# Optimization experiments

Measured on AMD Instinct MI355X. Metric: run time of the kernel, lower is better.

The kernel has to match this reference:

```python
import jax, jax.numpy as jnp
import numpy as np

N, D = 65536, 2000


def setup_inputs() -> dict:
    key = jax.random.key(0)
    factor = jax.random.normal(key, (N, D), dtype=jnp.float32)
    weight = jnp.float32(0.01)
    return {"factor": factor, "weight": weight}


def reference(factor, weight):
    # trace(factor[1:] @ factor[:-1].T) == sum of row-wise dot products of
    # shifted rows; O(n*d) instead of the original's O(n^2*d) matmul.
    n = factor.shape[0]
    tr = jnp.sum(factor[1:] * factor[:-1])
    return -weight * tr / (n - 1)
```

## Files before the change

kernel.cpp:

```cpp
#include <hip/hip_runtime.h>


#define N_ROWS 65536
#define D_COLS 2000
#define NBLOCKS 2048
#define NTHREADS 256
#define CHUNK 16000LL

__global__ __launch_bounds__(NTHREADS) void shifted_dot_kernel(
    const float* __restrict__ a,
    const float* __restrict__ weight,
    float* __restrict__ out,
    long long total4) {
    const float4* a4 = (const float4*)a;
    const long long shift4 = D_COLS / 4;

    long long start = (long long)blockIdx.x * CHUNK;
    long long end   = start + CHUNK;
    if (end > total4) end = total4;

    float acc = 0.0f;
    for (long long k = start + threadIdx.x; k < end; k += NTHREADS) {
        float4 x = a4[k];
        float4 y = a4[k + shift4];
        acc += x.x * y.x + x.y * y.y + x.z * y.z + x.w * y.w;
    }

    #pragma unroll
    for (int off = 32; off > 0; off >>= 1)
        acc += __shfl_down(acc, off, 64);

    __shared__ float wave_sums[NTHREADS / 64];
    int lane = threadIdx.x & 63;
    int wid  = threadIdx.x >> 6;
    if (lane == 0) wave_sums[wid] = acc;
    __syncthreads();

    if (threadIdx.x == 0) {
        float s = wave_sums[0] + wave_sums[1] + wave_sums[2] + wave_sums[3];
        float w = weight[0];
        atomicAdd(out, s * (-w / (float)(N_ROWS - 1)));
    }
}

extern "C" void kernel_launch(void* const* d_in, const int* in_sizes, int n_in,
                              void* d_out, int out_size, void* d_ws, size_t ws_size,
                              hipStream_t stream) {
    const float* factor = (const float*)d_in[0];
    const float* weight = (const float*)d_in[1];
    float* out = (float*)d_out;

    hipMemsetAsync(out, 0, sizeof(float), stream);

    const long long total4 = (long long)(N_ROWS - 1) * D_COLS / 4;

    dim3 grid(NBLOCKS), block(NTHREADS);
    shifted_dot_kernel<<<grid, block, 0, stream>>>(factor, weight, out, total4);
}
```

Before: 686.0 us.

## Walk columns down row bands and reuse previous row in registers

```diff
diff --git a/kernel.cpp b/kernel.cpp
--- a/kernel.cpp
+++ b/kernel.cpp
@@ -3,43 +3,57 @@
 
 #define N_ROWS 65536
 #define D_COLS 2000
-#define NBLOCKS 2048
-#define NTHREADS 256
-#define CHUNK 16000LL
+#define NBLOCKS 1024
+#define NTHREADS 512
+#define ROWS_PER_BLOCK 64
 
-__global__ __launch_bounds__(NTHREADS) void shifted_dot_kernel(
+__global__ __launch_bounds__(NTHREADS) void shifted_dot_colwise(
     const float* __restrict__ a,
     const float* __restrict__ weight,
-    float* __restrict__ out,
-    long long total4) {
-    const float4* a4 = (const float4*)a;
-    const long long shift4 = D_COLS / 4;
+    float* __restrict__ out) {
+    const int t = threadIdx.x;
 
-    long long start = (long long)blockIdx.x * CHUNK;
-    long long end   = start + CHUNK;
-    if (end > total4) end = total4;
+    float4 acc = make_float4(0.f, 0.f, 0.f, 0.f);
 
-    float acc = 0.0f;
-    for (long long k = start + threadIdx.x; k < end; k += NTHREADS) {
-        float4 x = a4[k];
-        float4 y = a4[k + shift4];
-        acc += x.x * y.x + x.y * y.y + x.z * y.z + x.w * y.w;
+    if (t < D_COLS / 4) {
+        const int r0 = blockIdx.x * ROWS_PER_BLOCK;
+        int r1 = r0 + ROWS_PER_BLOCK;
+        if (r1 > N_ROWS - 1) r1 = N_ROWS - 1;
+
+        const float4* col = (const float4*)(a + (long long)r0 * D_COLS) + t;
+        const int row4 = D_COLS / 4;
+
+        float4 prev = col[0];
+        #pragma unroll 4
+        for (int n = r0 + 1; n <= r1; ++n) {
+            col += row4;
+            float4 curr = *col;
+            acc.x += prev.x * curr.x;
+            acc.y += prev.y * curr.y;
+            acc.z += prev.z * curr.z;
+            acc.w += prev.w * curr.w;
+            prev = curr;
+        }
     }
+
+    float s = acc.x + acc.y + acc.z + acc.w;
 
     #pragma unroll
     for (int off = 32; off > 0; off >>= 1)
-        acc += __shfl_down(acc, off, 64);
+        s += __shfl_down(s, off, 64);
 
     __shared__ float wave_sums[NTHREADS / 64];
-    int lane = threadIdx.x & 63;
-    int wid  = threadIdx.x >> 6;
-    if (lane == 0) wave_sums[wid] = acc;
+    int lane = t & 63;
+    int wid  = t >> 6;
+    if (lane == 0) wave_sums[wid] = s;
     __syncthreads();
 
-    if (threadIdx.x == 0) {
-        float s = wave_sums[0] + wave_sums[1] + wave_sums[2] + wave_sums[3];
+    if (t == 0) {
+        float tot = 0.f;
+        #pragma unroll
+        for (int i = 0; i < NTHREADS / 64; ++i) tot += wave_sums[i];
         float w = weight[0];
-        atomicAdd(out, s * (-w / (float)(N_ROWS - 1)));
+        atomicAdd(out, tot * (-w / (float)(N_ROWS - 1)));
     }
 }
 
@@ -52,8 +66,6 @@
 
     hipMemsetAsync(out, 0, sizeof(float), stream);
 
-    const long long total4 = (long long)(N_ROWS - 1) * D_COLS / 4;
-
     dim3 grid(NBLOCKS), block(NTHREADS);
-    shifted_dot_kernel<<<grid, block, 0, stream>>>(factor, weight, out, total4);
+    shifted_dot_colwise<<<grid, block, 0, stream>>>(factor, weight, out);
 }
```

Measured after the change: 665.2 us. 3.0% less time.
